# Performance work log

Measured on AMD Instinct MI355X. Metric: run time of the kernel, lower is better.

Reference implementation:

```python
import jax, jax.numpy as jnp
import numpy as np

N1 = 64          # n1 (rows of matching matrix)
N2 = 64          # n2 (cols); N = n1*n2 association-graph nodes
N = N1 * N2
DENSITY = 0.15   # sparsity of affinity matrix K
CH = [64, 64, 64]
TAU = 0.05
SK_ITERS = 20


def _sinkhorn(s):
    # log-domain Sinkhorn, tau=0.05, 20 alternating row/col normalizations.
    # n1 == n2 here, so the dummy_row padding in the original is a no-op.
    log_s = s / TAU
    for i in range(SK_ITERS):
        log_s = log_s - jax.nn.logsumexp(log_s, axis=(1 if i % 2 == 0 else 0), keepdims=True)
    return jnp.exp(log_s)


def _lin(k, i, o, scale=0.1):
    kw, kb = jax.random.split(k)
    return (jax.random.normal(kw, (i, o), jnp.float32) * scale,
            jax.random.normal(kb, (o,), jnp.float32) * scale)


def setup_inputs() -> dict:
    key = jax.random.key(0)
    ks = jax.random.split(key, 16)
    mask = jax.random.uniform(ks[0], (N, N)) < DENSITY
    mask = mask | jnp.eye(N, dtype=bool)          # diag(K) supplies node features
    K = jnp.where(mask, jax.random.normal(ks[1], (N, N), jnp.float32), 0.0)
    # identical to torch: (K != 0).nonzero(as_tuple=False).t()
    edge_index = jnp.stack(jnp.nonzero(K)).astype(jnp.int32)
    inp = {"K": K, "edge_index": edge_index, "n1": N1, "n2": N2}
    dims_in = [1, CH[0], CH[1]]
    ki = 2
    for l in range(3):
        cw, cb = _lin(ks[ki], dims_in[l], CH[l]); ki += 1
        sw, sb = _lin(ks[ki], dims_in[l], CH[l]); ki += 1
        kw, kb = _lin(ks[ki], CH[l], 1); ki += 1
        inp.update({f"conv_w{l}": cw, f"conv_b{l}": cb,
                    f"self_w{l}": sw, f"self_b{l}": sb,
                    f"cls_w{l}": kw, f"cls_b{l}": kb})
    fw, fb = _lin(ks[ki], CH[2], 1)
    inp["fin_w"] = fw
    inp["fin_b"] = fb
    return inp


def _forward(K, edge_index, n1, n2, layer_params, fin_w, fin_b):
    n_nodes = n1 * n2
    src, dst = edge_index[0], edge_index[1]
    loop = jnp.arange(n_nodes, dtype=src.dtype)
    # PyG gcn_norm / add_remaining_self_loops: existing self-loop edges get
    # weight replaced (zeroed here, re-added with weight 1 below).
    w = jnp.concatenate([(src != dst).astype(K.dtype), jnp.ones((n_nodes,), K.dtype)])
    src_f = jnp.concatenate([src, loop])
    dst_f = jnp.concatenate([dst, loop])
    deg = jax.ops.segment_sum(w, dst_f, num_segments=n_nodes)
    dis = jnp.where(deg > 0, jax.lax.rsqrt(deg), 0.0)
    norm = dis[src_f] * w * dis[dst_f]                    # (E+N,)

    x = jnp.diag(K)[:, None]                              # (N, 1) node features
    for (cw, cb, sw, sb, kw, kb) in layer_params:
        xw = x @ cw                                       # (N, out)
        x_neigh = jax.ops.segment_sum(norm[:, None] * xw[src_f], dst_f,
                                      num_segments=n_nodes) + cb
        x_out = (x @ sw + sb) + x_neigh                   # self-loop + GCNConv
        sk = _sinkhorn((x_out @ kw + kb).reshape(n1, n2))
        x = x_out + sk.reshape(n_nodes, 1)                # broadcast over channels
    scores = x @ fin_w + fin_b                            # (N, 1)
    s = scores.reshape(n2, n1).T                          # (n1, n2)
    return _sinkhorn(s)


def reference(K, edge_index, n1, n2,
              conv_w0, conv_b0, self_w0, self_b0, cls_w0, cls_b0,
              conv_w1, conv_b1, self_w1, self_b1, cls_w1, cls_b1,
              conv_w2, conv_b2, self_w2, self_b2, cls_w2, cls_b2,
              fin_w, fin_b):
    layer_params = [(conv_w0, conv_b0, self_w0, self_b0, cls_w0, cls_b0),
                    (conv_w1, conv_b1, self_w1, self_b1, cls_w1, cls_b1),
                    (conv_w2, conv_b2, self_w2, self_b2, cls_w2, cls_b2)]
    return _forward(K, edge_index, n1, n2, layer_params, fin_w, fin_b)
```

## Files before the change

### kernel.cpp

```cpp
#include <hip/hip_runtime.h>
#include <hip/hip_bf16.h>
#include <cstdint>
#include <cstddef>

#define NN 4096

typedef float f32x4 __attribute__((ext_vector_type(4)));
typedef short s16x8 __attribute__((ext_vector_type(8)));

__device__ __forceinline__ float rdlane(float x, int lane) {
  return __int_as_float(__builtin_amdgcn_readlane(__float_as_int(x), lane));
}

__global__ __launch_bounds__(256) void k_prep(const float* __restrict__ K,
                                              unsigned long long* __restrict__ maskT) {
  const int lane = threadIdx.x & 63;
  const int wv = threadIdx.x >> 6;
  const int d0 = blockIdx.x * 256 + lane * 4;
  const int sbase = blockIdx.y * 256 + wv * 64;
  const int chunk = blockIdx.y * 4 + wv;
  unsigned long long w0 = 0, w1 = 0, w2 = 0, w3 = 0;
#pragma unroll 8
  for (int i = 0; i < 64; ++i) {
    const float4 kv = *(const float4*)(K + (size_t)(sbase + i) * NN + d0);
    w0 |= ((unsigned long long)(kv.x != 0.0f)) << i;
    w1 |= ((unsigned long long)(kv.y != 0.0f)) << i;
    w2 |= ((unsigned long long)(kv.z != 0.0f)) << i;
    w3 |= ((unsigned long long)(kv.w != 0.0f)) << i;
  }
  unsigned long long* mp = maskT + (size_t)chunk * NN + d0;
  mp[0] = w0; mp[1] = w1; mp[2] = w2; mp[3] = w3;
}

__device__ __forceinline__ void sinkhorn_reg(const float (&xR)[16], const float (&xC)[16],
    float& U, float& V, float* __restrict__ pp, int l, int w, int jb) {
  U = 0.f; V = 0.f;
#pragma unroll
  for (int it = 0; it < 20; ++it) {
    const bool row = (it & 1) == 0;
    float t[16];
#pragma unroll
    for (int j = 0; j < 16; ++j) {
      const float pot = rdlane(row ? V : U, jb + j);
      t[j] = (row ? xR[j] : xC[j]) - pot;
    }
    float a0 = fmaxf(t[0], t[1]),  a1 = fmaxf(t[2], t[3]);
    float a2 = fmaxf(t[4], t[5]),  a3 = fmaxf(t[6], t[7]);
    a0 = fmaxf(a0, fmaxf(t[8], t[9]));   a1 = fmaxf(a1, fmaxf(t[10], t[11]));
    a2 = fmaxf(a2, fmaxf(t[12], t[13])); a3 = fmaxf(a3, fmaxf(t[14], t[15]));
    const float mx = fmaxf(fmaxf(a0, a1), fmaxf(a2, a3));
    float s0 = 0.f, s1 = 0.f, s2 = 0.f, s3 = 0.f;
#pragma unroll
    for (int j = 0; j < 16; j += 4) {
      s0 += __expf(t[j] - mx);     s1 += __expf(t[j + 1] - mx);
      s2 += __expf(t[j + 2] - mx); s3 += __expf(t[j + 3] - mx);
    }
    const float sm = (s0 + s1) + (s2 + s3);
    float* buf = pp + (it & 1) * 768;
    buf[l * 12 + w] = mx;
    buf[l * 12 + 4 + w] = sm;
    __syncthreads();
    const f32x4 pm = *(const f32x4*)&buf[l * 12];
    const f32x4 ps = *(const f32x4*)&buf[l * 12 + 4];
    const float mM = fmaxf(fmaxf(pm[0], pm[1]), fmaxf(pm[2], pm[3]));
    const float ss = ps[0] * __expf(pm[0] - mM) + ps[1] * __expf(pm[1] - mM)
                   + ps[2] * __expf(pm[2] - mM) + ps[3] * __expf(pm[3] - mM);
    const float lse = mM + __logf(ss);
    if (row) U = lse; else V = lse;
  }
}

__global__ __launch_bounds__(256) void k_xform0(const float* __restrict__ K,
    const unsigned long long* __restrict__ maskT,
    const float* __restrict__ cw, const float* __restrict__ cb,
    const float* __restrict__ sw, const float* __restrict__ sb,
    float* __restrict__ disv,
    __hip_bfloat16* __restrict__ gHi, __hip_bfloat16* __restrict__ gLo,
    float* __restrict__ xselfT) {
  __shared__ float pdeg[4][64];
  const int lane = threadIdx.x & 63;
  const int wv = threadIdx.x >> 6;
  const int s = blockIdx.x * 64 + lane;
  unsigned cnt = 0;
#pragma unroll
  for (int q = 0; q < 16; ++q)
    cnt += (unsigned)__popcll(maskT[(size_t)(wv * 16 + q) * NN + s]);
  pdeg[wv][lane] = (float)cnt;
  __syncthreads();
  const float ds = rsqrtf(pdeg[0][lane] + pdeg[1][lane] + pdeg[2][lane] + pdeg[3][lane]);
  if (wv == 0) disv[s] = ds;
  const float xv = K[(size_t)s * NN + s];
#pragma unroll
  for (int i = 0; i < 16; ++i) {
    const int c = wv * 16 + i;
    const float gv = ds * xv * cw[c];
    const __hip_bfloat16 hi = __float2bfloat16(gv);
    gHi[(size_t)c * NN + s] = hi;
    gLo[(size_t)c * NN + s] = __float2bfloat16(gv - __bfloat162float(hi));
    xselfT[(size_t)c * NN + s] = xv * sw[c] + sb[c] + cb[c];
  }
}

__global__ __launch_bounds__(256, 1) void k_xform(const float* __restrict__ v,
    const float* __restrict__ vT,
    const float* __restrict__ xoutT, const float* __restrict__ disv,
    const float* __restrict__ cw, const float* __restrict__ cb,
    const float* __restrict__ sw, const float* __restrict__ sb,
    __hip_bfloat16* __restrict__ gHi, __hip_bfloat16* __restrict__ gLo,
    float* __restrict__ xselfT) {
  __shared__ __align__(16) float pp[2 * 768];
  __shared__ float xt[64][64];
  __shared__ float wcl[64 * 32], wsl[64 * 32];
  const int tid = threadIdx.x;
  const int l = tid & 63;
  const int w = tid >> 6;
  const int jb = w * 16;
  const int s = blockIdx.x * 64 + l;
  const int cbase = blockIdx.y * 32;
  float xR[16], xC[16];
#pragma unroll
  for (int q = 0; q < 4; ++q) {
    *(f32x4*)&xR[4 * q] = *(const f32x4*)&v[l * 64 + jb + 4 * q] * 20.0f;
    *(f32x4*)&xC[4 * q] = *(const f32x4*)&vT[l * 64 + jb + 4 * q] * 20.0f;
  }
#pragma unroll
  for (int r = 0; r < 16; ++r)
    xt[w * 16 + r][l] = xoutT[(size_t)(w * 16 + r) * NN + s];
#pragma unroll
  for (int q = 0; q < 8; ++q) {
    const int e = w * 512 + q * 64 + l;
    const int k = e >> 5, cl = e & 31;
    wcl[e] = cw[k * 64 + cbase + cl];
    wsl[e] = sw[k * 64 + cbase + cl];
  }
  float U, V;
  sinkhorn_reg(xR, xC, U, V, pp, l, w, jb);
  const int cl0 = w * 8;
  float accC[8], accS[8], csum[8], ssum[8];
#pragma unroll
  for (int i = 0; i < 8; ++i) { accC[i] = 0.f; accS[i] = 0.f; csum[i] = 0.f; ssum[i] = 0.f; }
  for (int k = 0; k < 64; ++k) {
    const float xv = xt[k][l];
    const f32x4 wcA = *(const f32x4*)&wcl[k * 32 + cl0];
    const f32x4 wcB = *(const f32x4*)&wcl[k * 32 + cl0 + 4];
    const f32x4 wsA = *(const f32x4*)&wsl[k * 32 + cl0];
    const f32x4 wsB = *(const f32x4*)&wsl[k * 32 + cl0 + 4];
#pragma unroll
    for (int i = 0; i < 4; ++i) {
      accC[i]     = fmaf(xv, wcA[i], accC[i]);     csum[i]     += wcA[i];
      accC[i + 4] = fmaf(xv, wcB[i], accC[i + 4]); csum[i + 4] += wcB[i];
      accS[i]     = fmaf(xv, wsA[i], accS[i]);     ssum[i]     += wsA[i];
      accS[i + 4] = fmaf(xv, wsB[i], accS[i + 4]); ssum[i + 4] += wsB[i];
    }
  }
  const int bx = blockIdx.x;
  const float skv = __expf(20.0f * v[bx * 64 + l] - rdlane(U, bx) - V);
  const float ds = disv[s];
#pragma unroll
  for (int i = 0; i < 8; ++i) {
    const int c = cbase + cl0 + i;
    const float gv = ds * (accC[i] + skv * csum[i]);
    const __hip_bfloat16 hi = __float2bfloat16(gv);
    gHi[(size_t)c * NN + s] = hi;
    gLo[(size_t)c * NN + s] = __float2bfloat16(gv - __bfloat162float(hi));
    xselfT[(size_t)c * NN + s] = accS[i] + skv * ssum[i] + sb[c] + cb[c];
  }
}

__global__ __launch_bounds__(512) void k_agg(const unsigned long long* __restrict__ maskT,
    const __hip_bfloat16* __restrict__ gHi, const __hip_bfloat16* __restrict__ gLo,
    const float* __restrict__ xselfT, const float* __restrict__ disv,
    const float* __restrict__ kw, const float* __restrict__ kb,
    const float* __restrict__ fw, const float* __restrict__ fb,
    float* __restrict__ xoutT, float* __restrict__ v, float* __restrict__ vT,
    float* __restrict__ sbF) {
  const int tid = threadIdx.x;
  const int lane = tid & 63;
  const int wv = tid >> 6;
  const int mtile = wv & 3;
  const int ks = wv >> 2;
  const int l15 = lane & 15;
  const int h = lane >> 4;
  const int d = blockIdx.x * 16 + l15;
  const int ch = mtile * 16 + l15;
  const short* __restrict__ gh = (const short*)gHi;
  const short* __restrict__ gl = (const short*)gLo;
  f32x4 acch = {0.f, 0.f, 0.f, 0.f};
  f32x4 accl = {0.f, 0.f, 0.f, 0.f};
  const int c0 = ks * 32;
#pragma unroll 4
  for (int c = c0; c < c0 + 32; ++c) {
    const unsigned long long w = maskT[(size_t)c * NN + d];
    const unsigned half0 = (unsigned)w, half1 = (unsigned)(w >> 32);
#pragma unroll
    for (int t = 0; t < 2; ++t) {
      const unsigned half = t ? half1 : half0;
      const unsigned hb = (half >> (8 * h)) & 0xFFu;
      s16x8 bfr;
#pragma unroll
      for (int j = 0; j < 8; ++j)
        bfr[j] = (short)(((hb >> j) & 1u) * 0x3F80u);
      const size_t abase = (size_t)ch * NN + (size_t)(c * 64 + t * 32 + 8 * h);
      const s16x8 ah = *(const s16x8*)(gh + abase);
      const s16x8 al = *(const s16x8*)(gl + abase);
      acch = __builtin_amdgcn_mfma_f32_16x16x32_bf16(ah, bfr, acch, 0, 0, 0);
      accl = __builtin_amdgcn_mfma_f32_16x16x32_bf16(al, bfr, accl, 0, 0, 0);
    }
  }
  __shared__ float rbuf[4][64][5];
  __shared__ float vred[16][17];
  __shared__ float vred2[16][17];
  f32x4 tot;
#pragma unroll
  for (int r = 0; r < 4; ++r) tot[r] = acch[r] + accl[r];
  if (ks == 1) {
#pragma unroll
    for (int r = 0; r < 4; ++r) rbuf[mtile][lane][r] = tot[r];
  }
  __syncthreads();
  if (ks == 0) {
    const float dd = disv[d];
    float p = 0.f, p2 = 0.f;
#pragma unroll
    for (int r = 0; r < 4; ++r) {
      const int chr = mtile * 16 + h * 4 + r;
      const float xo = xselfT[(size_t)chr * NN + d] + dd * (tot[r] + rbuf[mtile][lane][r]);
      xoutT[(size_t)chr * NN + d] = xo;
      p = fmaf(xo, kw[chr], p);
      p2 = fmaf(xo, fw[chr], p2);
    }
    vred[l15][mtile * 4 + h] = p;
    vred2[l15][mtile * 4 + h] = p2;
  }
  __syncthreads();
  if (tid < 16) {
    float sum = kb[0];
#pragma unroll
    for (int q = 0; q < 16; ++q) sum += vred[tid][q];
    const int d2 = blockIdx.x * 16 + tid;
    v[d2] = sum;
    vT[(d2 & 63) * 64 + (d2 >> 6)] = sum;
    if (sbF != nullptr) {
      float sum2 = fb[0];
#pragma unroll
      for (int q = 0; q < 16; ++q) sum2 += vred2[tid][q];
      sbF[d2] = sum2;
    }
  }
}

__global__ __launch_bounds__(256, 1) void k_final(const float* __restrict__ v,
    const float* __restrict__ vT, const float* __restrict__ sbF,
    const float* __restrict__ fw, float* __restrict__ out) {
  __shared__ __align__(16) float pp[2 * 768];
  __shared__ __align__(16) float scR[64 * 68];
  __shared__ __align__(16) float scT[64 * 68];
  __shared__ float fwl[64];
  const int tid = threadIdx.x;
  const int l = tid & 63;
  const int w = tid >> 6;
  const int jb = w * 16;
  float xR[16], xC[16];
#pragma unroll
  for (int q = 0; q < 4; ++q) {
    *(f32x4*)&xR[4 * q] = *(const f32x4*)&v[l * 64 + jb + 4 * q] * 20.0f;
    *(f32x4*)&xC[4 * q] = *(const f32x4*)&vT[l * 64 + jb + 4 * q] * 20.0f;
  }
  if (tid < 64) fwl[tid] = fw[tid];
  float U1, V1;
  sinkhorn_reg(xR, xC, U1, V1, pp, l, w, jb);
  float sumw = 0.f;
#pragma unroll
  for (int k = 0; k < 64; ++k) sumw += fwl[k];
#pragma unroll
  for (int k = 0; k < 16; ++k) {
    const int n = k * 256 + tid;
    const int r2 = 4 * k + w;
    const float sk2 = __expf(20.0f * v[n] - rdlane(U1, r2) - V1);
    const float val = (sbF[n] + sk2 * sumw) * 20.0f;
    scR[l * 68 + r2] = val;
    scT[r2 * 68 + l] = val;
  }
  __syncthreads();
#pragma unroll
  for (int q = 0; q < 4; ++q) {
    *(f32x4*)&xR[4 * q] = *(const f32x4*)&scR[l * 68 + jb + 4 * q];
    *(f32x4*)&xC[4 * q] = *(const f32x4*)&scT[l * 68 + jb + 4 * q];
  }
  float U2, V2;
  sinkhorn_reg(xR, xC, U2, V2, pp, l, w, jb);
#pragma unroll
  for (int q = 0; q < 16; ++q) {
    const int e = q * 256 + tid;
    const int i1 = 4 * q + w;
    out[e] = __expf(scR[i1 * 68 + l] - rdlane(U2, i1) - V2);
  }
}

extern "C" void kernel_launch(void* const* d_in, const int* in_sizes, int n_in,
                              void* d_out, int out_size, void* d_ws, size_t ws_size,
                              hipStream_t stream) {
  const float* K = (const float*)d_in[0];
  const float* cw[3] = {(const float*)d_in[4],  (const float*)d_in[10], (const float*)d_in[16]};
  const float* cb[3] = {(const float*)d_in[5],  (const float*)d_in[11], (const float*)d_in[17]};
  const float* sw[3] = {(const float*)d_in[6],  (const float*)d_in[12], (const float*)d_in[18]};
  const float* sb[3] = {(const float*)d_in[7],  (const float*)d_in[13], (const float*)d_in[19]};
  const float* kw[3] = {(const float*)d_in[8],  (const float*)d_in[14], (const float*)d_in[20]};
  const float* kb[3] = {(const float*)d_in[9],  (const float*)d_in[15], (const float*)d_in[21]};
  const float* fw = (const float*)d_in[22];
  const float* fb = (const float*)d_in[23];
  float* out = (float*)d_out;

  char* ws = (char*)d_ws;
  const size_t KB = 1024, MB = 1024 * 1024;
  float* disv               = (float*)(ws + 0);
  float* v                  = (float*)(ws + 16 * KB);
  float* vT                 = (float*)(ws + 32 * KB);
  float* sbF                = (float*)(ws + 48 * KB);
  unsigned long long* maskT = (unsigned long long*)(ws + 64 * KB);
  __hip_bfloat16* gHi       = (__hip_bfloat16*)(ws + 64 * KB + 2 * MB);
  __hip_bfloat16* gLo       = (__hip_bfloat16*)(ws + 64 * KB + 2 * MB + 512 * KB);
  float* xselfT             = (float*)(ws + 64 * KB + 3 * MB);
  float* xoutT              = (float*)(ws + 64 * KB + 4 * MB);
  (void)in_sizes; (void)n_in; (void)out_size; (void)ws_size;

  k_prep<<<dim3(16, 16), 256, 0, stream>>>(K, maskT);
  k_xform0<<<64, 256, 0, stream>>>(K, maskT, cw[0], cb[0], sw[0], sb[0],
                                   disv, gHi, gLo, xselfT);
  k_agg<<<256, 512, 0, stream>>>(maskT, gHi, gLo, xselfT, disv, kw[0], kb[0],
                                 fw, fb, xoutT, v, vT, nullptr);
  for (int l = 1; l < 3; ++l) {
    k_xform<<<dim3(64, 2), 256, 0, stream>>>(v, vT, xoutT, disv, cw[l], cb[l], sw[l], sb[l],
                                             gHi, gLo, xselfT);
    k_agg<<<256, 512, 0, stream>>>(maskT, gHi, gLo, xselfT, disv, kw[l], kb[l],
                                   fw, fb, xoutT, v, vT, (l == 2) ? sbF : nullptr);
  }
  k_final<<<1, 256, 0, stream>>>(v, vT, sbF, fw, out);
}
```

Before: 197.7 us.

## Run Sinkhorn in a single wavefront, overlapping it with the xform matmul waves

The Sinkhorn normalization is rewritten so one 64-lane wavefront holds a full row and column in registers. That removes the per-iteration block barriers and LDS partial reductions that came from splitting the work across four waves. In k_xform a dedicated wave runs Sinkhorn while four other waves run the 64x64 transform concurrently, and the block grows to 320 threads. k_final drops to a single wave and reads a transposed copy of the final scores written by k_agg, so it no longer rebuilds a transposed tile in shared memory. The cost is longer serial per-lane loops and high register pressure from two 64-float arrays, which may cause spills.

New measurement: 235.0 us. +18.9%, slower.

```diff
diff --git a/kernel.cpp b/kernel.cpp
--- a/kernel.cpp
+++ b/kernel.cpp
@@ -7,10 +7,6 @@
 
 typedef float f32x4 __attribute__((ext_vector_type(4)));
 typedef short s16x8 __attribute__((ext_vector_type(8)));
-
-__device__ __forceinline__ float rdlane(float x, int lane) {
-  return __int_as_float(__builtin_amdgcn_readlane(__float_as_int(x), lane));
-}
 
 __global__ __launch_bounds__(256) void k_prep(const float* __restrict__ K,
                                               unsigned long long* __restrict__ maskT) {
@@ -32,40 +28,44 @@
   mp[0] = w0; mp[1] = w1; mp[2] = w2; mp[3] = w3;
 }
 
-__device__ __forceinline__ void sinkhorn_reg(const float (&xR)[16], const float (&xC)[16],
-    float& U, float& V, float* __restrict__ pp, int l, int w, int jb) {
+__device__ __forceinline__ void sinkhorn_w1(const float (&xR)[64], const float (&xC)[64],
+    float& U, float& V, float* __restrict__ pot, int l) {
   U = 0.f; V = 0.f;
-#pragma unroll
+#pragma unroll 1
   for (int it = 0; it < 20; ++it) {
     const bool row = (it & 1) == 0;
-    float t[16];
-#pragma unroll
-    for (int j = 0; j < 16; ++j) {
-      const float pot = rdlane(row ? V : U, jb + j);
-      t[j] = (row ? xR[j] : xC[j]) - pot;
-    }
-    float a0 = fmaxf(t[0], t[1]),  a1 = fmaxf(t[2], t[3]);
-    float a2 = fmaxf(t[4], t[5]),  a3 = fmaxf(t[6], t[7]);
-    a0 = fmaxf(a0, fmaxf(t[8], t[9]));   a1 = fmaxf(a1, fmaxf(t[10], t[11]));
-    a2 = fmaxf(a2, fmaxf(t[12], t[13])); a3 = fmaxf(a3, fmaxf(t[14], t[15]));
-    const float mx = fmaxf(fmaxf(a0, a1), fmaxf(a2, a3));
+    pot[l] = row ? V : U;
+    asm volatile("s_waitcnt lgkmcnt(0)" ::: "memory");
+    float t[64];
+    if (row) {
+#pragma unroll
+      for (int q = 0; q < 16; ++q) {
+        const f32x4 p = *(const f32x4*)&pot[4 * q];
+#pragma unroll
+        for (int i = 0; i < 4; ++i) t[4 * q + i] = xR[4 * q + i] - p[i];
+      }
+    } else {
+#pragma unroll
+      for (int q = 0; q < 16; ++q) {
+        const f32x4 p = *(const f32x4*)&pot[4 * q];
+#pragma unroll
+        for (int i = 0; i < 4; ++i) t[4 * q + i] = xC[4 * q + i] - p[i];
+      }
+    }
+    float m0 = t[0], m1 = t[1], m2 = t[2], m3 = t[3];
+#pragma unroll
+    for (int j = 4; j < 64; j += 4) {
+      m0 = fmaxf(m0, t[j]);     m1 = fmaxf(m1, t[j + 1]);
+      m2 = fmaxf(m2, t[j + 2]); m3 = fmaxf(m3, t[j + 3]);
+    }
+    const float mx = fmaxf(fmaxf(m0, m1), fmaxf(m2, m3));
     float s0 = 0.f, s1 = 0.f, s2 = 0.f, s3 = 0.f;
 #pragma unroll
-    for (int j = 0; j < 16; j += 4) {
+    for (int j = 0; j < 64; j += 4) {
       s0 += __expf(t[j] - mx);     s1 += __expf(t[j + 1] - mx);
       s2 += __expf(t[j + 2] - mx); s3 += __expf(t[j + 3] - mx);
     }
-    const float sm = (s0 + s1) + (s2 + s3);
-    float* buf = pp + (it & 1) * 768;
-    buf[l * 12 + w] = mx;
-    buf[l * 12 + 4 + w] = sm;
-    __syncthreads();
-    const f32x4 pm = *(const f32x4*)&buf[l * 12];
-    const f32x4 ps = *(const f32x4*)&buf[l * 12 + 4];
-    const float mM = fmaxf(fmaxf(pm[0], pm[1]), fmaxf(pm[2], pm[3]));
-    const float ss = ps[0] * __expf(pm[0] - mM) + ps[1] * __expf(pm[1] - mM)
-                   + ps[2] * __expf(pm[2] - mM) + ps[3] * __expf(pm[3] - mM);
-    const float lse = mM + __logf(ss);
+    const float lse = mx + __logf((s0 + s1) + (s2 + s3));
     if (row) U = lse; else V = lse;
   }
 }
@@ -101,69 +101,83 @@
   }
 }
 
-__global__ __launch_bounds__(256, 1) void k_xform(const float* __restrict__ v,
+__global__ __launch_bounds__(320, 2) void k_xform(const float* __restrict__ v,
     const float* __restrict__ vT,
     const float* __restrict__ xoutT, const float* __restrict__ disv,
     const float* __restrict__ cw, const float* __restrict__ cb,
     const float* __restrict__ sw, const float* __restrict__ sb,
     __hip_bfloat16* __restrict__ gHi, __hip_bfloat16* __restrict__ gLo,
     float* __restrict__ xselfT) {
-  __shared__ __align__(16) float pp[2 * 768];
+  __shared__ __align__(16) float pot[64];
+  __shared__ __align__(16) float uW[64], vW[64];
   __shared__ float xt[64][64];
   __shared__ float wcl[64 * 32], wsl[64 * 32];
   const int tid = threadIdx.x;
   const int l = tid & 63;
   const int w = tid >> 6;
-  const int jb = w * 16;
   const int s = blockIdx.x * 64 + l;
   const int cbase = blockIdx.y * 32;
-  float xR[16], xC[16];
-#pragma unroll
-  for (int q = 0; q < 4; ++q) {
-    *(f32x4*)&xR[4 * q] = *(const f32x4*)&v[l * 64 + jb + 4 * q] * 20.0f;
-    *(f32x4*)&xC[4 * q] = *(const f32x4*)&vT[l * 64 + jb + 4 * q] * 20.0f;
-  }
-#pragma unroll
-  for (int r = 0; r < 16; ++r)
-    xt[w * 16 + r][l] = xoutT[(size_t)(w * 16 + r) * NN + s];
-#pragma unroll
-  for (int q = 0; q < 8; ++q) {
-    const int e = w * 512 + q * 64 + l;
-    const int k = e >> 5, cl = e & 31;
-    wcl[e] = cw[k * 64 + cbase + cl];
-    wsl[e] = sw[k * 64 + cbase + cl];
-  }
-  float U, V;
-  sinkhorn_reg(xR, xC, U, V, pp, l, w, jb);
-  const int cl0 = w * 8;
+  float xR[64], xC[64];
+  if (w == 0) {
+#pragma unroll
+    for (int q = 0; q < 16; ++q) {
+      *(f32x4*)&xR[4 * q] = *(const f32x4*)&v[l * 64 + 4 * q] * 20.0f;
+      *(f32x4*)&xC[4 * q] = *(const f32x4*)&vT[l * 64 + 4 * q] * 20.0f;
+    }
+  } else {
+    const int ww = w - 1;
+#pragma unroll
+    for (int r = 0; r < 16; ++r)
+      xt[ww * 16 + r][l] = xoutT[(size_t)(ww * 16 + r) * NN + s];
+#pragma unroll
+    for (int q = 0; q < 8; ++q) {
+      const int e = ww * 512 + q * 64 + l;
+      const int k = e >> 5, cl = e & 31;
+      wcl[e] = cw[k * 64 + cbase + cl];
+      wsl[e] = sw[k * 64 + cbase + cl];
+    }
+  }
+  __syncthreads();
   float accC[8], accS[8], csum[8], ssum[8];
-#pragma unroll
-  for (int i = 0; i < 8; ++i) { accC[i] = 0.f; accS[i] = 0.f; csum[i] = 0.f; ssum[i] = 0.f; }
-  for (int k = 0; k < 64; ++k) {
-    const float xv = xt[k][l];
-    const f32x4 wcA = *(const f32x4*)&wcl[k * 32 + cl0];
-    const f32x4 wcB = *(const f32x4*)&wcl[k * 32 + cl0 + 4];
-    const f32x4 wsA = *(const f32x4*)&wsl[k * 32 + cl0];
-    const f32x4 wsB = *(const f32x4*)&wsl[k * 32 + cl0 + 4];
-#pragma unroll
-    for (int i = 0; i < 4; ++i) {
-      accC[i]     = fmaf(xv, wcA[i], accC[i]);     csum[i]     += wcA[i];
-      accC[i + 4] = fmaf(xv, wcB[i], accC[i + 4]); csum[i + 4] += wcB[i];
-      accS[i]     = fmaf(xv, wsA[i], accS[i]);     ssum[i]     += wsA[i];
-      accS[i + 4] = fmaf(xv, wsB[i], accS[i + 4]); ssum[i + 4] += wsB[i];
-    }
-  }
-  const int bx = blockIdx.x;
-  const float skv = __expf(20.0f * v[bx * 64 + l] - rdlane(U, bx) - V);
-  const float ds = disv[s];
-#pragma unroll
-  for (int i = 0; i < 8; ++i) {
-    const int c = cbase + cl0 + i;
-    const float gv = ds * (accC[i] + skv * csum[i]);
-    const __hip_bfloat16 hi = __float2bfloat16(gv);
-    gHi[(size_t)c * NN + s] = hi;
-    gLo[(size_t)c * NN + s] = __float2bfloat16(gv - __bfloat162float(hi));
-    xselfT[(size_t)c * NN + s] = accS[i] + skv * ssum[i] + sb[c] + cb[c];
+  if (w == 0) {
+    float U, V;
+    sinkhorn_w1(xR, xC, U, V, pot, l);
+    uW[l] = U; vW[l] = V;
+    asm volatile("s_waitcnt lgkmcnt(0)" ::: "memory");
+  } else {
+    const int cl0 = (w - 1) * 8;
+#pragma unroll
+    for (int i = 0; i < 8; ++i) { accC[i] = 0.f; accS[i] = 0.f; csum[i] = 0.f; ssum[i] = 0.f; }
+    for (int k = 0; k < 64; ++k) {
+      const float xv = xt[k][l];
+      const f32x4 wcA = *(const f32x4*)&wcl[k * 32 + cl0];
+      const f32x4 wcB = *(const f32x4*)&wcl[k * 32 + cl0 + 4];
+      const f32x4 wsA = *(const f32x4*)&wsl[k * 32 + cl0];
+      const f32x4 wsB = *(const f32x4*)&wsl[k * 32 + cl0 + 4];
+#pragma unroll
+      for (int i = 0; i < 4; ++i) {
+        accC[i]     = fmaf(xv, wcA[i], accC[i]);     csum[i]     += wcA[i];
+        accC[i + 4] = fmaf(xv, wcB[i], accC[i + 4]); csum[i + 4] += wcB[i];
+        accS[i]     = fmaf(xv, wsA[i], accS[i]);     ssum[i]     += wsA[i];
+        accS[i + 4] = fmaf(xv, wsB[i], accS[i + 4]); ssum[i + 4] += wsB[i];
+      }
+    }
+  }
+  __syncthreads();
+  if (w > 0) {
+    const int bx = blockIdx.x;
+    const float skv = __expf(20.0f * v[bx * 64 + l] - uW[bx] - vW[l]);
+    const float ds = disv[s];
+    const int cl0 = (w - 1) * 8;
+#pragma unroll
+    for (int i = 0; i < 8; ++i) {
+      const int c = cbase + cl0 + i;
+      const float gv = ds * (accC[i] + skv * csum[i]);
+      const __hip_bfloat16 hi = __float2bfloat16(gv);
+      gHi[(size_t)c * NN + s] = hi;
+      gLo[(size_t)c * NN + s] = __float2bfloat16(gv - __bfloat162float(hi));
+      xselfT[(size_t)c * NN + s] = accS[i] + skv * ssum[i] + sb[c] + cb[c];
+    }
   }
 }
 
@@ -173,7 +187,7 @@
     const float* __restrict__ kw, const float* __restrict__ kb,
     const float* __restrict__ fw, const float* __restrict__ fb,
     float* __restrict__ xoutT, float* __restrict__ v, float* __restrict__ vT,
-    float* __restrict__ sbF) {
+    float* __restrict__ sbF, float* __restrict__ sbFT) {
   const int tid = threadIdx.x;
   const int lane = tid & 63;
   const int wv = tid >> 6;
@@ -245,55 +259,54 @@
 #pragma unroll
       for (int q = 0; q < 16; ++q) sum2 += vred2[tid][q];
       sbF[d2] = sum2;
-    }
-  }
-}
-
-__global__ __launch_bounds__(256, 1) void k_final(const float* __restrict__ v,
+      sbFT[(d2 & 63) * 64 + (d2 >> 6)] = sum2;
+    }
+  }
+}
+
+__global__ __launch_bounds__(64, 1) void k_final(const float* __restrict__ v,
     const float* __restrict__ vT, const float* __restrict__ sbF,
-    const float* __restrict__ fw, float* __restrict__ out) {
-  __shared__ __align__(16) float pp[2 * 768];
-  __shared__ __align__(16) float scR[64 * 68];
-  __shared__ __align__(16) float scT[64 * 68];
-  __shared__ float fwl[64];
-  const int tid = threadIdx.x;
-  const int l = tid & 63;
-  const int w = tid >> 6;
-  const int jb = w * 16;
-  float xR[16], xC[16];
-#pragma unroll
-  for (int q = 0; q < 4; ++q) {
-    *(f32x4*)&xR[4 * q] = *(const f32x4*)&v[l * 64 + jb + 4 * q] * 20.0f;
-    *(f32x4*)&xC[4 * q] = *(const f32x4*)&vT[l * 64 + jb + 4 * q] * 20.0f;
-  }
-  if (tid < 64) fwl[tid] = fw[tid];
+    const float* __restrict__ sbFT, const float* __restrict__ fw,
+    float* __restrict__ out) {
+  __shared__ __align__(16) float potA[64], potB[64];
+  const int l = threadIdx.x;
+  float xR[64], xC[64];
+#pragma unroll
+  for (int q = 0; q < 16; ++q) {
+    *(f32x4*)&xR[4 * q] = *(const f32x4*)&v[l * 64 + 4 * q] * 20.0f;
+    *(f32x4*)&xC[4 * q] = *(const f32x4*)&vT[l * 64 + 4 * q] * 20.0f;
+  }
+  float sumw = 0.f;
+#pragma unroll
+  for (int k = 0; k < 64; ++k) sumw += fw[k];
   float U1, V1;
-  sinkhorn_reg(xR, xC, U1, V1, pp, l, w, jb);
-  float sumw = 0.f;
-#pragma unroll
-  for (int k = 0; k < 64; ++k) sumw += fwl[k];
-#pragma unroll
-  for (int k = 0; k < 16; ++k) {
-    const int n = k * 256 + tid;
-    const int r2 = 4 * k + w;
-    const float sk2 = __expf(20.0f * v[n] - rdlane(U1, r2) - V1);
-    const float val = (sbF[n] + sk2 * sumw) * 20.0f;
-    scR[l * 68 + r2] = val;
-    scT[r2 * 68 + l] = val;
-  }
-  __syncthreads();
-#pragma unroll
-  for (int q = 0; q < 4; ++q) {
-    *(f32x4*)&xR[4 * q] = *(const f32x4*)&scR[l * 68 + jb + 4 * q];
-    *(f32x4*)&xC[4 * q] = *(const f32x4*)&scT[l * 68 + jb + 4 * q];
+  sinkhorn_w1(xR, xC, U1, V1, potA, l);
+  potA[l] = U1; potB[l] = V1;
+  asm volatile("s_waitcnt lgkmcnt(0)" ::: "memory");
+#pragma unroll
+  for (int q = 0; q < 16; ++q) {
+    const f32x4 Ub = *(const f32x4*)&potA[4 * q];
+    const f32x4 Vb = *(const f32x4*)&potB[4 * q];
+    const f32x4 sT = *(const f32x4*)&sbFT[l * 64 + 4 * q];
+    const f32x4 sF = *(const f32x4*)&sbF[l * 64 + 4 * q];
+#pragma unroll
+    for (int i = 0; i < 4; ++i) {
+      const int j = 4 * q + i;
+      const float a = xR[j], b = xC[j];
+      xR[j] = (sT[i] + __expf(b - Ub[i] - V1) * sumw) * 20.0f;
+      xC[j] = (sF[i] + __expf(a - U1 - Vb[i]) * sumw) * 20.0f;
+    }
   }
   float U2, V2;
-  sinkhorn_reg(xR, xC, U2, V2, pp, l, w, jb);
+  sinkhorn_w1(xR, xC, U2, V2, potA, l);
+  potA[l] = U2;
+  asm volatile("s_waitcnt lgkmcnt(0)" ::: "memory");
 #pragma unroll
   for (int q = 0; q < 16; ++q) {
-    const int e = q * 256 + tid;
-    const int i1 = 4 * q + w;
-    out[e] = __expf(scR[i1 * 68 + l] - rdlane(U2, i1) - V2);
+    const f32x4 Ub = *(const f32x4*)&potA[4 * q];
+#pragma unroll
+    for (int i = 0; i < 4; ++i)
+      out[(4 * q + i) * 64 + l] = __expf(xC[4 * q + i] - Ub[i] - V2);
   }
 }
 
@@ -322,18 +335,20 @@
   __hip_bfloat16* gLo       = (__hip_bfloat16*)(ws + 64 * KB + 2 * MB + 512 * KB);
   float* xselfT             = (float*)(ws + 64 * KB + 3 * MB);
   float* xoutT              = (float*)(ws + 64 * KB + 4 * MB);
+  float* sbFT               = (float*)(ws + 64 * KB + 5 * MB);
   (void)in_sizes; (void)n_in; (void)out_size; (void)ws_size;
 
   k_prep<<<dim3(16, 16), 256, 0, stream>>>(K, maskT);
   k_xform0<<<64, 256, 0, stream>>>(K, maskT, cw[0], cb[0], sw[0], sb[0],
                                    disv, gHi, gLo, xselfT);
   k_agg<<<256, 512, 0, stream>>>(maskT, gHi, gLo, xselfT, disv, kw[0], kb[0],
-                                 fw, fb, xoutT, v, vT, nullptr);
+                                 fw, fb, xoutT, v, vT, nullptr, nullptr);
   for (int l = 1; l < 3; ++l) {
-    k_xform<<<dim3(64, 2), 256, 0, stream>>>(v, vT, xoutT, disv, cw[l], cb[l], sw[l], sb[l],
+    k_xform<<<dim3(64, 2), 320, 0, stream>>>(v, vT, xoutT, disv, cw[l], cb[l], sw[l], sb[l],
                                              gHi, gLo, xselfT);
     k_agg<<<256, 512, 0, stream>>>(maskT, gHi, gLo, xselfT, disv, kw[l], kb[l],
-                                   fw, fb, xoutT, v, vT, (l == 2) ? sbF : nullptr);
-  }
-  k_final<<<1, 256, 0, stream>>>(v, vT, sbF, fw, out);
-}
+                                   fw, fb, xoutT, v, vT,
+                                   (l == 2) ? sbF : nullptr, (l == 2) ? sbFT : nullptr);
+  }
+  k_final<<<1, 64, 0, stream>>>(v, vT, sbF, sbFT, fw, out);
+}
```

## Rework Sinkhorn reduction to quad shuffles and drop k_agg split-K

Applied to the files above, without the earlier changes.

Sinkhorn now assigns each row to four lanes of a quad, reduces max and sum with xor shuffles, and exchanges potentials through small shared arrays instead of per-lane readlane plus a 4-wave LSE merge. k_agg no longer splits the 64 mask chunks across two wave groups. Each block instead covers 32 destination columns with the full reduction, which removes the partial-sum shared buffer and one barrier. The trade-off is half as many k_agg blocks, each with a longer serial loop, which cuts parallelism on a GPU with many CUs.

Measured after the change: 281.4 us. +42.3%, slower.

```diff
diff --git a/kernel.cpp b/kernel.cpp
--- a/kernel.cpp
+++ b/kernel.cpp
@@ -7,10 +7,6 @@
 
 typedef float f32x4 __attribute__((ext_vector_type(4)));
 typedef short s16x8 __attribute__((ext_vector_type(8)));
-
-__device__ __forceinline__ float rdlane(float x, int lane) {
-  return __int_as_float(__builtin_amdgcn_readlane(__float_as_int(x), lane));
-}
 
 __global__ __launch_bounds__(256) void k_prep(const float* __restrict__ K,
                                               unsigned long long* __restrict__ maskT) {
@@ -32,41 +28,43 @@
   mp[0] = w0; mp[1] = w1; mp[2] = w2; mp[3] = w3;
 }
 
-__device__ __forceinline__ void sinkhorn_reg(const float (&xR)[16], const float (&xC)[16],
-    float& U, float& V, float* __restrict__ pp, int l, int w, int jb) {
-  U = 0.f; V = 0.f;
-#pragma unroll
+__device__ __forceinline__ void sinkhorn_q(const float (&xR)[16], const float (&xC)[16],
+    float* __restrict__ uArr, float* __restrict__ vArr, int l, int w) {
+  const int q4 = (l & 3) * 16;
+  const int g = w * 16 + (l >> 2);
+  if (w == 0) vArr[l] = 0.0f;
+  __syncthreads();
+#pragma unroll 1
   for (int it = 0; it < 20; ++it) {
     const bool row = (it & 1) == 0;
+    const float* pot = row ? vArr : uArr;
     float t[16];
 #pragma unroll
-    for (int j = 0; j < 16; ++j) {
-      const float pot = rdlane(row ? V : U, jb + j);
-      t[j] = (row ? xR[j] : xC[j]) - pot;
+    for (int qq = 0; qq < 4; ++qq) {
+      const f32x4 p = *(const f32x4*)&pot[q4 + 4 * qq];
+#pragma unroll
+      for (int i = 0; i < 4; ++i)
+        t[4 * qq + i] = (row ? xR[4 * qq + i] : xC[4 * qq + i]) - p[i];
     }
     float a0 = fmaxf(t[0], t[1]),  a1 = fmaxf(t[2], t[3]);
     float a2 = fmaxf(t[4], t[5]),  a3 = fmaxf(t[6], t[7]);
     a0 = fmaxf(a0, fmaxf(t[8], t[9]));   a1 = fmaxf(a1, fmaxf(t[10], t[11]));
     a2 = fmaxf(a2, fmaxf(t[12], t[13])); a3 = fmaxf(a3, fmaxf(t[14], t[15]));
-    const float mx = fmaxf(fmaxf(a0, a1), fmaxf(a2, a3));
+    float mx = fmaxf(fmaxf(a0, a1), fmaxf(a2, a3));
+    mx = fmaxf(mx, __shfl_xor(mx, 1));
+    mx = fmaxf(mx, __shfl_xor(mx, 2));
     float s0 = 0.f, s1 = 0.f, s2 = 0.f, s3 = 0.f;
 #pragma unroll
     for (int j = 0; j < 16; j += 4) {
       s0 += __expf(t[j] - mx);     s1 += __expf(t[j + 1] - mx);
       s2 += __expf(t[j + 2] - mx); s3 += __expf(t[j + 3] - mx);
     }
-    const float sm = (s0 + s1) + (s2 + s3);
-    float* buf = pp + (it & 1) * 768;
-    buf[l * 12 + w] = mx;
-    buf[l * 12 + 4 + w] = sm;
+    float sm = (s0 + s1) + (s2 + s3);
+    sm += __shfl_xor(sm, 1);
+    sm += __shfl_xor(sm, 2);
+    const float lse = mx + __logf(sm);
+    if ((l & 3) == 0) (row ? uArr : vArr)[g] = lse;
     __syncthreads();
-    const f32x4 pm = *(const f32x4*)&buf[l * 12];
-    const f32x4 ps = *(const f32x4*)&buf[l * 12 + 4];
-    const float mM = fmaxf(fmaxf(pm[0], pm[1]), fmaxf(pm[2], pm[3]));
-    const float ss = ps[0] * __expf(pm[0] - mM) + ps[1] * __expf(pm[1] - mM)
-                   + ps[2] * __expf(pm[2] - mM) + ps[3] * __expf(pm[3] - mM);
-    const float lse = mM + __logf(ss);
-    if (row) U = lse; else V = lse;
   }
 }
 
@@ -108,20 +106,20 @@
     const float* __restrict__ sw, const float* __restrict__ sb,
     __hip_bfloat16* __restrict__ gHi, __hip_bfloat16* __restrict__ gLo,
     float* __restrict__ xselfT) {
-  __shared__ __align__(16) float pp[2 * 768];
+  __shared__ __align__(16) float uArr[64], vArr[64];
   __shared__ float xt[64][64];
   __shared__ float wcl[64 * 32], wsl[64 * 32];
   const int tid = threadIdx.x;
   const int l = tid & 63;
   const int w = tid >> 6;
-  const int jb = w * 16;
   const int s = blockIdx.x * 64 + l;
   const int cbase = blockIdx.y * 32;
+  const int srow = (w * 16 + (l >> 2)) * 64 + (l & 3) * 16;
   float xR[16], xC[16];
 #pragma unroll
   for (int q = 0; q < 4; ++q) {
-    *(f32x4*)&xR[4 * q] = *(const f32x4*)&v[l * 64 + jb + 4 * q] * 20.0f;
-    *(f32x4*)&xC[4 * q] = *(const f32x4*)&vT[l * 64 + jb + 4 * q] * 20.0f;
+    *(f32x4*)&xR[4 * q] = *(const f32x4*)&v[srow + 4 * q] * 20.0f;
+    *(f32x4*)&xC[4 * q] = *(const f32x4*)&vT[srow + 4 * q] * 20.0f;
   }
 #pragma unroll
   for (int r = 0; r < 16; ++r)
@@ -133,8 +131,7 @@
     wcl[e] = cw[k * 64 + cbase + cl];
     wsl[e] = sw[k * 64 + cbase + cl];
   }
-  float U, V;
-  sinkhorn_reg(xR, xC, U, V, pp, l, w, jb);
+  sinkhorn_q(xR, xC, uArr, vArr, l, w);
   const int cl0 = w * 8;
   float accC[8], accS[8], csum[8], ssum[8];
 #pragma unroll
@@ -154,7 +151,7 @@
     }
   }
   const int bx = blockIdx.x;
-  const float skv = __expf(20.0f * v[bx * 64 + l] - rdlane(U, bx) - V);
+  const float skv = __expf(20.0f * v[bx * 64 + l] - uArr[bx] - vArr[l]);
   const float ds = disv[s];
 #pragma unroll
   for (int i = 0; i < 8; ++i) {
@@ -178,18 +175,17 @@
   const int lane = tid & 63;
   const int wv = tid >> 6;
   const int mtile = wv & 3;
-  const int ks = wv >> 2;
+  const int nhalf = wv >> 2;
   const int l15 = lane & 15;
   const int h = lane >> 4;
-  const int d = blockIdx.x * 16 + l15;
+  const int d = blockIdx.x * 32 + nhalf * 16 + l15;
   const int ch = mtile * 16 + l15;
   const short* __restrict__ gh = (const short*)gHi;
   const short* __restrict__ gl = (const short*)gLo;
   f32x4 acch = {0.f, 0.f, 0.f, 0.f};
   f32x4 accl = {0.f, 0.f, 0.f, 0.f};
-  const int c0 = ks * 32;
 #pragma unroll 4
-  for (int c = c0; c < c0 + 32; ++c) {
+  for (int c = 0; c < 64; ++c) {
     const unsigned long long w = maskT[(size_t)c * NN + d];
     const unsigned half0 = (unsigned)w, half1 = (unsigned)(w >> 32);
 #pragma unroll
@@ -207,43 +203,33 @@
       accl = __builtin_amdgcn_mfma_f32_16x16x32_bf16(al, bfr, accl, 0, 0, 0);
     }
   }
-  __shared__ float rbuf[4][64][5];
-  __shared__ float vred[16][17];
-  __shared__ float vred2[16][17];
-  f32x4 tot;
-#pragma unroll
-  for (int r = 0; r < 4; ++r) tot[r] = acch[r] + accl[r];
-  if (ks == 1) {
-#pragma unroll
-    for (int r = 0; r < 4; ++r) rbuf[mtile][lane][r] = tot[r];
-  }
+  __shared__ float vred[2][16][17];
+  __shared__ float vred2[2][16][17];
+  const float dd = disv[d];
+  float p = 0.f, p2 = 0.f;
+#pragma unroll
+  for (int r = 0; r < 4; ++r) {
+    const int chr = mtile * 16 + h * 4 + r;
+    const float xo = xselfT[(size_t)chr * NN + d] + dd * (acch[r] + accl[r]);
+    xoutT[(size_t)chr * NN + d] = xo;
+    p = fmaf(xo, kw[chr], p);
+    p2 = fmaf(xo, fw[chr], p2);
+  }
+  vred[nhalf][l15][mtile * 4 + h] = p;
+  vred2[nhalf][l15][mtile * 4 + h] = p2;
   __syncthreads();
-  if (ks == 0) {
-    const float dd = disv[d];
-    float p = 0.f, p2 = 0.f;
-#pragma unroll
-    for (int r = 0; r < 4; ++r) {
-      const int chr = mtile * 16 + h * 4 + r;
-      const float xo = xselfT[(size_t)chr * NN + d] + dd * (tot[r] + rbuf[mtile][lane][r]);
-      xoutT[(size_t)chr * NN + d] = xo;
-      p = fmaf(xo, kw[chr], p);
-      p2 = fmaf(xo, fw[chr], p2);
-    }
-    vred[l15][mtile * 4 + h] = p;
-    vred2[l15][mtile * 4 + h] = p2;
-  }
-  __syncthreads();
-  if (tid < 16) {
+  if (tid < 32) {
+    const int nh = tid >> 4, dl = tid & 15;
     float sum = kb[0];
 #pragma unroll
-    for (int q = 0; q < 16; ++q) sum += vred[tid][q];
-    const int d2 = blockIdx.x * 16 + tid;
+    for (int q = 0; q < 16; ++q) sum += vred[nh][dl][q];
+    const int d2 = blockIdx.x * 32 + tid;
     v[d2] = sum;
     vT[(d2 & 63) * 64 + (d2 >> 6)] = sum;
     if (sbF != nullptr) {
       float sum2 = fb[0];
 #pragma unroll
-      for (int q = 0; q < 16; ++q) sum2 += vred2[tid][q];
+      for (int q = 0; q < 16; ++q) sum2 += vred2[nh][dl][q];
       sbF[d2] = sum2;
     }
   }
@@ -252,23 +238,22 @@
 __global__ __launch_bounds__(256, 1) void k_final(const float* __restrict__ v,
     const float* __restrict__ vT, const float* __restrict__ sbF,
     const float* __restrict__ fw, float* __restrict__ out) {
-  __shared__ __align__(16) float pp[2 * 768];
+  __shared__ __align__(16) float uArr[64], vArr[64];
   __shared__ __align__(16) float scR[64 * 68];
   __shared__ __align__(16) float scT[64 * 68];
   __shared__ float fwl[64];
   const int tid = threadIdx.x;
   const int l = tid & 63;
   const int w = tid >> 6;
-  const int jb = w * 16;
+  const int srow = (w * 16 + (l >> 2)) * 64 + (l & 3) * 16;
   float xR[16], xC[16];
 #pragma unroll
   for (int q = 0; q < 4; ++q) {
-    *(f32x4*)&xR[4 * q] = *(const f32x4*)&v[l * 64 + jb + 4 * q] * 20.0f;
-    *(f32x4*)&xC[4 * q] = *(const f32x4*)&vT[l * 64 + jb + 4 * q] * 20.0f;
+    *(f32x4*)&xR[4 * q] = *(const f32x4*)&v[srow + 4 * q] * 20.0f;
+    *(f32x4*)&xC[4 * q] = *(const f32x4*)&vT[srow + 4 * q] * 20.0f;
   }
   if (tid < 64) fwl[tid] = fw[tid];
-  float U1, V1;
-  sinkhorn_reg(xR, xC, U1, V1, pp, l, w, jb);
+  sinkhorn_q(xR, xC, uArr, vArr, l, w);
   float sumw = 0.f;
 #pragma unroll
   for (int k = 0; k < 64; ++k) sumw += fwl[k];
@@ -276,7 +261,7 @@
   for (int k = 0; k < 16; ++k) {
     const int n = k * 256 + tid;
     const int r2 = 4 * k + w;
-    const float sk2 = __expf(20.0f * v[n] - rdlane(U1, r2) - V1);
+    const float sk2 = __expf(20.0f * v[n] - uArr[r2] - vArr[l]);
     const float val = (sbF[n] + sk2 * sumw) * 20.0f;
     scR[l * 68 + r2] = val;
     scT[r2 * 68 + l] = val;
@@ -284,16 +269,16 @@
   __syncthreads();
 #pragma unroll
   for (int q = 0; q < 4; ++q) {
-    *(f32x4*)&xR[4 * q] = *(const f32x4*)&scR[l * 68 + jb + 4 * q];
-    *(f32x4*)&xC[4 * q] = *(const f32x4*)&scT[l * 68 + jb + 4 * q];
-  }
-  float U2, V2;
-  sinkhorn_reg(xR, xC, U2, V2, pp, l, w, jb);
+    const int base = (w * 16 + (l >> 2)) * 68 + (l & 3) * 16 + 4 * q;
+    *(f32x4*)&xR[4 * q] = *(const f32x4*)&scR[base];
+    *(f32x4*)&xC[4 * q] = *(const f32x4*)&scT[base];
+  }
+  sinkhorn_q(xR, xC, uArr, vArr, l, w);
 #pragma unroll
   for (int q = 0; q < 16; ++q) {
     const int e = q * 256 + tid;
     const int i1 = 4 * q + w;
-    out[e] = __expf(scR[i1 * 68 + l] - rdlane(U2, i1) - V2);
+    out[e] = __expf(scR[i1 * 68 + l] - uArr[i1] - vArr[l]);
   }
 }
 
@@ -327,12 +312,12 @@
   k_prep<<<dim3(16, 16), 256, 0, stream>>>(K, maskT);
   k_xform0<<<64, 256, 0, stream>>>(K, maskT, cw[0], cb[0], sw[0], sb[0],
                                    disv, gHi, gLo, xselfT);
-  k_agg<<<256, 512, 0, stream>>>(maskT, gHi, gLo, xselfT, disv, kw[0], kb[0],
+  k_agg<<<128, 512, 0, stream>>>(maskT, gHi, gLo, xselfT, disv, kw[0], kb[0],
                                  fw, fb, xoutT, v, vT, nullptr);
   for (int l = 1; l < 3; ++l) {
     k_xform<<<dim3(64, 2), 256, 0, stream>>>(v, vT, xoutT, disv, cw[l], cb[l], sw[l], sb[l],
                                              gHi, gLo, xselfT);
-    k_agg<<<256, 512, 0, stream>>>(maskT, gHi, gLo, xselfT, disv, kw[l], kb[l],
+    k_agg<<<128, 512, 0, stream>>>(maskT, gHi, gLo, xselfT, disv, kw[l], kb[l],
                                    fw, fb, xoutT, v, vT, (l == 2) ? sbF : nullptr);
   }
   k_final<<<1, 256, 0, stream>>>(v, vT, sbF, fw, out);
```
